# Kernel tuning notes

Measured on AMD Instinct MI355X. Metric: run time of the kernel, lower is better.

## Reference

```python
import jax, jax.numpy as jnp
import numpy as np

B, S, HID, NH = 2, 2048, 1024, 16
HD = HID // NH  # head_dim = 64


def setup_inputs() -> dict:
    key = jax.random.key(0)
    ks = jax.random.split(key, 11)
    sc = 1.0 / np.sqrt(HID)
    inp = {
        "query": jax.random.normal(ks[0], (B, S, HID), jnp.float32),
        "key_": jax.random.normal(ks[1], (B, S, HID), jnp.float32),
        "value": jax.random.normal(ks[2], (B, S, HID), jnp.float32),
        "Wq": jax.random.normal(ks[3], (HID, HID), jnp.float32) * sc,
        "bq": jnp.zeros((HID,), jnp.float32),
        "Wk": jax.random.normal(ks[4], (HID, HID), jnp.float32) * sc,
        "bk": jnp.zeros((HID,), jnp.float32),
        "Wv": jax.random.normal(ks[5], (HID, HID), jnp.float32) * sc,
        "bv": jnp.zeros((HID,), jnp.float32),
        "Wo": jax.random.normal(ks[6], (HID, HID), jnp.float32) * sc,
        "bo": jnp.zeros((HID,), jnp.float32),
    }
    return inp


def _split_heads(x):
    # [B, S, HID] -> [B, NH, S, HD]
    return x.reshape(B, S, NH, HD).transpose(0, 2, 1, 3)


def reference(query, key_, value, Wq, bq, Wk, bk, Wv, bv, Wo, bo):
    q = _split_heads(query @ Wq + bq)
    k = _split_heads(key_ @ Wk + bk)
    v = _split_heads(value @ Wv + bv)
    scale = 1.0 / jnp.sqrt(jnp.asarray(HD, q.dtype))
    # [B, NH, S, S] scores (unfused attention, as in the original module)
    scores = jnp.einsum("bhqd,bhkd->bhqk", q, k) * scale
    attn = jax.nn.softmax(scores, axis=-1)
    ctx = jnp.einsum("bhqk,bhkd->bhqd", attn, v)  # [B, NH, S, HD]
    ctx = ctx.transpose(0, 2, 1, 3).reshape(B, S, HID)
    return ctx @ Wo + bo
```

## Files before the change

kernel.cpp:

```cpp
#include <hip/hip_runtime.h>


typedef unsigned short u16;
typedef unsigned int u32;
typedef __bf16 bf16x8 __attribute__((ext_vector_type(8)));
typedef float f32x4 __attribute__((ext_vector_type(4)));
typedef u16 u16x4 __attribute__((ext_vector_type(4)));

__device__ __forceinline__ u16 f2bf(float f) {
  __bf16 h = (__bf16)f;
  return *(u16*)&h;
}

__device__ __forceinline__ void gll16(const void* g, void* l) {
  __builtin_amdgcn_global_load_lds(
      (const __attribute__((address_space(1))) u32*)g,
      (__attribute__((address_space(3))) u32*)l, 16, 0, 0);
}

__global__ __launch_bounds__(256) void prep_kernel(
    const float* __restrict__ q32, const float* __restrict__ k32,
    const float* __restrict__ v32,
    u16* __restrict__ qb, u16* __restrict__ kb, u16* __restrict__ vb,
    const float* __restrict__ W0, const float* __restrict__ W1,
    const float* __restrict__ W2, const float* __restrict__ W3,
    u16* __restrict__ T0, u16* __restrict__ T1,
    u16* __restrict__ T2, u16* __restrict__ T3) {
  int blk = blockIdx.x, tid = threadIdx.x;
  if (blk < 12288) {
    int which = blk >> 12;
    const float* in = (which == 0) ? q32 : (which == 1) ? k32 : v32;
    u16* out = (which == 0) ? qb : (which == 1) ? kb : vb;
    int i = (blk & 4095) * 256 + tid;
    float4 v = ((const float4*)in)[i];
    u16x4 o;
    o.x = f2bf(v.x); o.y = f2bf(v.y); o.z = f2bf(v.z); o.w = f2bf(v.w);
    ((u16x4*)out)[i] = o;
  } else {
    int tb = blk - 12288;
    int z = tb >> 10, rest = tb & 1023;
    const float* W = (z == 0) ? W0 : (z == 1) ? W1 : (z == 2) ? W2 : W3;
    u16* WT = (z == 0) ? T0 : (z == 1) ? T1 : (z == 2) ? T2 : T3;
    __shared__ float t[32][33];
    int bx = (rest & 31) * 32, by = (rest >> 5) * 32;
    int tx = tid & 31, ty = tid >> 5;
#pragma unroll
    for (int i = ty; i < 32; i += 8) t[i][tx] = W[(by + i) * 1024 + bx + tx];
    __syncthreads();
#pragma unroll
    for (int i = ty; i < 32; i += 8) WT[(bx + i) * 1024 + by + tx] = f2bf(t[tx][i]);
  }
}

struct GemmJob {
  const u16* A; const u16* BT; const float* bias;
  float* Cf; u16* Cb; int mode; float oscale;
};

template <int BN>
__global__ __launch_bounds__(256, 4) void gemm_sbuf(GemmJob j0, GemmJob j1, GemmJob j2) {
  constexpr int NT = BN / 32;
  constexpr int NBC = BN / 32;
  const int K = 1024, N = 1024;
  __shared__ __align__(16) u16 As[128 * 64];
  __shared__ __align__(16) u16 Bs[BN * 64];
  int blk = blockIdx.x, tid = threadIdx.x;
  int z, r0, bm, bn;
  if (BN == 128) {
    z = blk >> 8; r0 = blk & 255;
    int xcd = r0 & 7, i5 = r0 >> 3;
    bm = (xcd * 4 + (i5 & 3)) * 128;
    bn = (i5 >> 2) * 128;
  } else {
    z = 0; r0 = blk;
    int xcd = r0 & 7, i6 = r0 >> 3;
    bm = (xcd * 4 + (i6 & 3)) * 128;
    bn = (i6 >> 2) * 64;
  }
  GemmJob j = (z == 0) ? j0 : (z == 1) ? j1 : j2;
  int w = tid >> 6, lane = tid & 63, quad = lane >> 4, l16 = lane & 15;
  int wr = (w >> 1) * 64, wc = (w & 1) * (BN / 2);
  f32x4 acc[4][NT] = {};

  auto stage = [&](int kk) {
#pragma unroll
    for (int i = 0; i < 4; ++i) {
      int c = tid + i * 256;
      int r = c >> 3, jp = c & 7, jg = jp ^ (r & 7);
      gll16(&j.A[(size_t)(bm + r) * K + kk + jg * 8], &As[c * 8]);
    }
#pragma unroll
    for (int i = 0; i < NBC; ++i) {
      int c = tid + i * 256;
      int r = c >> 3, jp = c & 7, jg = jp ^ (r & 7);
      gll16(&j.BT[(size_t)(bn + r) * K + kk + jg * 8], &Bs[c * 8]);
    }
  };

  for (int it = 0; it < 16; ++it) {
    __syncthreads();
    stage(it * 64);
    __syncthreads();
#pragma unroll
    for (int ks = 0; ks < 2; ++ks) {
      bf16x8 af[4], bfr[NT];
#pragma unroll
      for (int mt = 0; mt < 4; ++mt) {
        int row = wr + mt * 16 + l16;
        af[mt] = *(const bf16x8*)&As[row * 64 + (((ks * 4 + quad) ^ (row & 7))) * 8];
      }
#pragma unroll
      for (int nt = 0; nt < NT; ++nt) {
        int row = wc + nt * 16 + l16;
        bfr[nt] = *(const bf16x8*)&Bs[row * 64 + (((ks * 4 + quad) ^ (row & 7))) * 8];
      }
#pragma unroll
      for (int mt = 0; mt < 4; ++mt)
#pragma unroll
        for (int nt = 0; nt < NT; ++nt)
          acc[mt][nt] = __builtin_amdgcn_mfma_f32_16x16x32_bf16(af[mt], bfr[nt], acc[mt][nt], 0, 0, 0);
    }
  }

#pragma unroll
  for (int mt = 0; mt < 4; ++mt)
#pragma unroll
    for (int nt = 0; nt < NT; ++nt)
#pragma unroll
      for (int r = 0; r < 4; ++r) {
        int row = bm + wr + mt * 16 + quad * 4 + r;
        int col = bn + wc + nt * 16 + l16;
        float v = (acc[mt][nt][r] + j.bias[col]) * j.oscale;
        if (j.mode == 0) {
          j.Cf[(size_t)row * N + col] = v;
        } else {
          int b = row >> 11, s = row & 2047, h = col >> 6, d = col & 63;
          u16 bv = f2bf(v);
          if (j.mode == 1)
            j.Cb[(((size_t)(b * 16 + h) * 2048 + s) << 6) + d] = bv;
          else
            j.Cb[((size_t)(b * 16 + h) * 64 + d) * 2048 + s] = bv;
        }
      }
}

__global__ __launch_bounds__(512, 4) void attn_kernel(
    const u16* __restrict__ Q,
    const u16* __restrict__ Kk,
    const u16* __restrict__ VT,
    u16* __restrict__ ctx)
{
  __shared__ __align__(16) u16 Ks[2][2][64 * 64];
  __shared__ __align__(16) u16 Vs[2][2][64 * 64];

  int blk = blockIdx.x;
  int qt = (blk >> 3) & 15;
  int bh = (blk & 7) * 4 + (blk >> 7);
  int b = bh >> 4, h = bh & 15;
  const u16* Qb = Q + ((size_t)bh * 2048 + qt * 128) * 64;
  const u16* Kb = Kk + (size_t)bh * 2048 * 64;
  const u16* Vb = VT + (size_t)bh * 64 * 2048;
  int tid = threadIdx.x, w = tid >> 6, lane = tid & 63, quad = lane >> 4, l16 = lane & 15;
  int g = tid >> 8;
  int wl = w & 3;
  int tt = tid & 255;
  int rowbase = wl * 32;

  bf16x8 qf[2][2];
#pragma unroll
  for (int f = 0; f < 2; ++f)
#pragma unroll
    for (int ks = 0; ks < 2; ++ks)
      qf[f][ks] = *(const bf16x8*)&Qb[(rowbase + f * 16 + l16) * 64 + ks * 32 + quad * 8];

  f32x4 Oacc[2][4] = {};
  float lacc0 = 0.f, lacc1 = 0.f;

  int c0 = tt, c1 = tt + 256;
  int kr0 = c0 >> 3, kj0 = (c0 & 7) ^ (kr0 & 7);
  int kr1 = c1 >> 3, kj1 = (c1 & 7) ^ (kr1 & 7);
  const u16* ksrc0 = Kb + (size_t)(g * 1024 + kr0) * 64 + kj0 * 8;
  const u16* ksrc1 = Kb + (size_t)(g * 1024 + kr1) * 64 + kj1 * 8;
  const u16* vsrc0 = Vb + (size_t)kr0 * 2048 + g * 1024 + kj0 * 8;
  const u16* vsrc1 = Vb + (size_t)kr1 * 2048 + g * 1024 + kj1 * 8;
  u16* kdst0 = &Ks[g][0][c0 * 8];
  u16* kdst1 = &Ks[g][0][c1 * 8];
  u16* vdst0 = &Vs[g][0][c0 * 8];
  u16* vdst1 = &Vs[g][0][c1 * 8];

  u32 koff[2][2][2];
  u32 voff[2][4];
#pragma unroll
  for (int c = 0; c < 2; ++c) {
#pragma unroll
    for (int nt2 = 0; nt2 < 2; ++nt2)
#pragma unroll
      for (int ks = 0; ks < 2; ++ks)
        koff[c][nt2][ks] = ((c * 2 + nt2) * 16 + l16) * 64 +
                           (((ks * 4 + quad) ^ (l16 & 7)) * 8);
#pragma unroll
    for (int dt = 0; dt < 4; ++dt)
      voff[c][dt] = (dt * 16 + l16) * 64 + ((((c * 4 + quad) ^ (l16 & 7))) * 8);
  }
  const u16* kbase = &Ks[g][0][0];
  const u16* vbase = &Vs[g][0][0];

  gll16(ksrc0, kdst0); gll16(ksrc1, kdst1);
  gll16(vsrc0, vdst0); gll16(vsrc1, vdst1);
  __syncthreads();

  for (int kv = 0; kv < 16; ++kv) {
    int cur = kv & 1;
    if (kv < 15) {
      ksrc0 += 64 * 64; ksrc1 += 64 * 64;
      vsrc0 += 64;      vsrc1 += 64;
      u32 so = (cur ^ 1) * (64 * 64);
      gll16(ksrc0, kdst0 + so); gll16(ksrc1, kdst1 + so);
      gll16(vsrc0, vdst0 + so); gll16(vsrc1, vdst1 + so);
    }
    u32 bo = cur * (64 * 64);
    const u16* kb = kbase + bo;
    const u16* vb = vbase + bo;

#pragma unroll
    for (int c = 0; c < 2; ++c) {
      f32x4 Sc[2][2] = {};
      __builtin_amdgcn_s_setprio(1);
#pragma unroll
      for (int nt2 = 0; nt2 < 2; ++nt2) {
#pragma unroll
        for (int ks = 0; ks < 2; ++ks) {
          bf16x8 kfr = *(const bf16x8*)(kb + koff[c][nt2][ks]);
          Sc[0][nt2] = __builtin_amdgcn_mfma_f32_16x16x32_bf16(kfr, qf[0][ks], Sc[0][nt2], 0, 0, 0);
          Sc[1][nt2] = __builtin_amdgcn_mfma_f32_16x16x32_bf16(kfr, qf[1][ks], Sc[1][nt2], 0, 0, 0);
        }
      }
      __builtin_amdgcn_s_setprio(0);

      bf16x8 pf[2];
#pragma unroll
      for (int f = 0; f < 2; ++f) {
        float p0 = __builtin_amdgcn_exp2f(Sc[f][0][0]);
        float p1 = __builtin_amdgcn_exp2f(Sc[f][0][1]);
        float p2 = __builtin_amdgcn_exp2f(Sc[f][0][2]);
        float p3 = __builtin_amdgcn_exp2f(Sc[f][0][3]);
        float p4 = __builtin_amdgcn_exp2f(Sc[f][1][0]);
        float p5 = __builtin_amdgcn_exp2f(Sc[f][1][1]);
        float p6 = __builtin_amdgcn_exp2f(Sc[f][1][2]);
        float p7 = __builtin_amdgcn_exp2f(Sc[f][1][3]);
        float ls = ((p0 + p1) + (p2 + p3)) + ((p4 + p5) + (p6 + p7));
        if (f == 0) lacc0 += ls; else lacc1 += ls;
        u32 u0, u1, u2, u3;
        asm("v_cvt_pk_bf16_f32 %0, %1, %2" : "=v"(u0) : "v"(p0), "v"(p1));
        asm("v_cvt_pk_bf16_f32 %0, %1, %2" : "=v"(u1) : "v"(p2), "v"(p3));
        asm("v_cvt_pk_bf16_f32 %0, %1, %2" : "=v"(u2) : "v"(p4), "v"(p5));
        asm("v_cvt_pk_bf16_f32 %0, %1, %2" : "=v"(u3) : "v"(p6), "v"(p7));
        asm("v_permlane32_swap_b32 %0, %1" : "+v"(u0), "+v"(u2));
        asm("v_permlane32_swap_b32 %0, %1" : "+v"(u1), "+v"(u3));
        asm("v_permlane16_swap_b32 %0, %1" : "+v"(u0), "+v"(u2));
        asm("v_permlane16_swap_b32 %0, %1" : "+v"(u1), "+v"(u3));
        union { u32 u[4]; bf16x8 v; } cv;
        cv.u[0] = u0; cv.u[1] = u1; cv.u[2] = u2; cv.u[3] = u3;
        pf[f] = cv.v;
      }

      __builtin_amdgcn_s_setprio(1);
#pragma unroll
      for (int dt = 0; dt < 4; ++dt) {
        bf16x8 vf = *(const bf16x8*)(vb + voff[c][dt]);
        Oacc[0][dt] = __builtin_amdgcn_mfma_f32_16x16x32_bf16(vf, pf[0], Oacc[0][dt], 0, 0, 0);
        Oacc[1][dt] = __builtin_amdgcn_mfma_f32_16x16x32_bf16(vf, pf[1], Oacc[1][dt], 0, 0, 0);
      }
      __builtin_amdgcn_s_setprio(0);
    }

    __syncthreads();
  }

  float lred[2];
#pragma unroll
  for (int f = 0; f < 2; ++f) {
    float l = (f == 0) ? lacc0 : lacc1;
    l += __shfl_xor(l, 16, 64);
    l += __shfl_xor(l, 32, 64);
    lred[f] = l;
  }

  float* ox = (float*)&Ks[0][0][0];
  float* lx = (float*)&Vs[0][0][0];
  if (g == 1) {
#pragma unroll
    for (int f = 0; f < 2; ++f) {
#pragma unroll
      for (int dt = 0; dt < 4; ++dt) {
        int jc = (dt * 4 + quad) ^ l16;
        *(f32x4*)&ox[(size_t)(rowbase + f * 16 + l16) * 64 + jc * 4] = Oacc[f][dt];
      }
      if (quad == 0) lx[rowbase + f * 16 + l16] = lred[f];
    }
  }
  __syncthreads();
  if (g == 0) {
#pragma unroll
    for (int f = 0; f < 2; ++f) {
      float lt = lred[f] + lx[rowbase + f * 16 + l16];
      float linv = 1.0f / lt;
      int s = qt * 128 + rowbase + f * 16 + l16;
#pragma unroll
      for (int dt = 0; dt < 4; ++dt) {
        int jc = (dt * 4 + quad) ^ l16;
        f32x4 o1 = *(const f32x4*)&ox[(size_t)(rowbase + f * 16 + l16) * 64 + jc * 4];
        u16x4 o;
#pragma unroll
        for (int r = 0; r < 4; ++r) o[r] = f2bf((Oacc[f][dt][r] + o1[r]) * linv);
        *(u16x4*)&ctx[(size_t)(b * 2048 + s) * 1024 + h * 64 + dt * 16 + quad * 4] = o;
      }
    }
  }
}


extern "C" void kernel_launch(void* const* d_in, const int* in_sizes, int n_in,
                              void* d_out, int out_size, void* d_ws, size_t ws_size,
                              hipStream_t stream) {
  const float* query = (const float*)d_in[0];
  const float* key_  = (const float*)d_in[1];
  const float* value = (const float*)d_in[2];
  const float* Wq = (const float*)d_in[3];
  const float* bq = (const float*)d_in[4];
  const float* Wk = (const float*)d_in[5];
  const float* bk = (const float*)d_in[6];
  const float* Wv = (const float*)d_in[7];
  const float* bv = (const float*)d_in[8];
  const float* Wo = (const float*)d_in[9];
  const float* bo = (const float*)d_in[10];
  float* out = (float*)d_out;

  char* ws = (char*)d_ws;
  const size_t MB = 1024 * 1024;
  u16* Aq  = (u16*)(ws + 0 * MB);
  u16* Ak  = (u16*)(ws + 8 * MB);
  u16* Av  = (u16*)(ws + 16 * MB);
  u16* WqT = (u16*)(ws + 24 * MB);
  u16* WkT = (u16*)(ws + 26 * MB);
  u16* WvT = (u16*)(ws + 28 * MB);
  u16* WoT = (u16*)(ws + 30 * MB);
  u16* Qp  = (u16*)(ws + 32 * MB);
  u16* Kp  = (u16*)(ws + 40 * MB);
  u16* VTp = (u16*)(ws + 48 * MB);
  u16* Ctx = (u16*)(ws + 56 * MB);

  prep_kernel<<<16384, 256, 0, stream>>>(query, key_, value, Aq, Ak, Av,
                                         Wq, Wk, Wv, Wo, WqT, WkT, WvT, WoT);

  const float sc = 0.125f * 1.44269504f;
  GemmJob jq{Aq, WqT, bq, nullptr, Qp, 1, sc};
  GemmJob jk{Ak, WkT, bk, nullptr, Kp, 1, 1.0f};
  GemmJob jv{Av, WvT, bv, nullptr, VTp, 2, 1.0f};
  gemm_sbuf<128><<<768, 256, 0, stream>>>(jq, jk, jv);

  attn_kernel<<<512, 512, 0, stream>>>(Qp, Kp, VTp, Ctx);

  GemmJob jo{Ctx, WoT, bo, out, nullptr, 0, 1.0f};
  gemm_sbuf<64><<<512, 256, 0, stream>>>(jo, jo, jo);
}
```

Baseline: 225.6 us.

## Split attention KV sequence across four wave groups with 1024-thread blocks

Doubles the attention block to 1024 threads and splits the key/value sequence into four 512-key groups instead of two, each streaming 32-key tiles with double-buffered async loads into LDS. The partial output accumulators and row sums are combined through a two-stage LDS tree reduction before normalisation and the bf16 store. This raises the number of waves in flight to hide memory and MFMA latency. It costs an extra reduction stage with more barriers, smaller tiles with more loop iterations, and register pressure under the tighter launch bounds.

```diff
diff --git a/kernel.cpp b/kernel.cpp
--- a/kernel.cpp
+++ b/kernel.cpp
@@ -144,14 +144,14 @@
       }
 }
 
-__global__ __launch_bounds__(512, 4) void attn_kernel(
+__global__ __launch_bounds__(1024, 4) void attn_kernel(
     const u16* __restrict__ Q,
     const u16* __restrict__ Kk,
     const u16* __restrict__ VT,
     u16* __restrict__ ctx)
 {
-  __shared__ __align__(16) u16 Ks[2][2][64 * 64];
-  __shared__ __align__(16) u16 Vs[2][2][64 * 64];
+  __shared__ __align__(16) u16 Ks[4][2][32 * 64];
+  __shared__ __align__(16) u16 Vs[4][2][64 * 32];
 
   int blk = blockIdx.x;
   int qt = (blk >> 3) & 15;
@@ -160,9 +160,9 @@
   const u16* Qb = Q + ((size_t)bh * 2048 + qt * 128) * 64;
   const u16* Kb = Kk + (size_t)bh * 2048 * 64;
   const u16* Vb = VT + (size_t)bh * 64 * 2048;
-  int tid = threadIdx.x, w = tid >> 6, lane = tid & 63, quad = lane >> 4, l16 = lane & 15;
+  int tid = threadIdx.x, lane = tid & 63, quad = lane >> 4, l16 = lane & 15;
   int g = tid >> 8;
-  int wl = w & 3;
+  int wl = (tid >> 6) & 3;
   int tt = tid & 255;
   int rowbase = wl * 32;
 
@@ -176,103 +176,91 @@
   f32x4 Oacc[2][4] = {};
   float lacc0 = 0.f, lacc1 = 0.f;
 
-  int c0 = tt, c1 = tt + 256;
-  int kr0 = c0 >> 3, kj0 = (c0 & 7) ^ (kr0 & 7);
-  int kr1 = c1 >> 3, kj1 = (c1 & 7) ^ (kr1 & 7);
-  const u16* ksrc0 = Kb + (size_t)(g * 1024 + kr0) * 64 + kj0 * 8;
-  const u16* ksrc1 = Kb + (size_t)(g * 1024 + kr1) * 64 + kj1 * 8;
-  const u16* vsrc0 = Vb + (size_t)kr0 * 2048 + g * 1024 + kj0 * 8;
-  const u16* vsrc1 = Vb + (size_t)kr1 * 2048 + g * 1024 + kj1 * 8;
-  u16* kdst0 = &Ks[g][0][c0 * 8];
-  u16* kdst1 = &Ks[g][0][c1 * 8];
-  u16* vdst0 = &Vs[g][0][c0 * 8];
-  u16* vdst1 = &Vs[g][0][c1 * 8];
-
-  u32 koff[2][2][2];
-  u32 voff[2][4];
-#pragma unroll
-  for (int c = 0; c < 2; ++c) {
-#pragma unroll
-    for (int nt2 = 0; nt2 < 2; ++nt2)
-#pragma unroll
-      for (int ks = 0; ks < 2; ++ks)
-        koff[c][nt2][ks] = ((c * 2 + nt2) * 16 + l16) * 64 +
-                           (((ks * 4 + quad) ^ (l16 & 7)) * 8);
-#pragma unroll
-    for (int dt = 0; dt < 4; ++dt)
-      voff[c][dt] = (dt * 16 + l16) * 64 + ((((c * 4 + quad) ^ (l16 & 7))) * 8);
-  }
+  int kr = tt >> 3, kjp = tt & 7, kjg = kjp ^ (kr & 7);
+  int vd = tt >> 2, vjp = tt & 3, vjg = vjp ^ (vd & 3);
+  const u16* ksrc = Kb + (size_t)(g * 512 + kr) * 64 + kjg * 8;
+  const u16* vsrc = Vb + (size_t)vd * 2048 + g * 512 + vjg * 8;
+  u16* kdst = &Ks[g][0][tt * 8];
+  u16* vdst = &Vs[g][0][tt * 8];
+
+  u32 koff[2][2];
+#pragma unroll
+  for (int nt2 = 0; nt2 < 2; ++nt2)
+#pragma unroll
+    for (int ks = 0; ks < 2; ++ks)
+      koff[nt2][ks] = (nt2 * 16 + l16) * 64 + (((ks * 4 + quad) ^ (l16 & 7)) * 8);
+  u32 voff[4];
+#pragma unroll
+  for (int dt = 0; dt < 4; ++dt)
+    voff[dt] = (dt * 16 + l16) * 32 + ((quad ^ (l16 & 3)) * 8);
   const u16* kbase = &Ks[g][0][0];
   const u16* vbase = &Vs[g][0][0];
 
-  gll16(ksrc0, kdst0); gll16(ksrc1, kdst1);
-  gll16(vsrc0, vdst0); gll16(vsrc1, vdst1);
+  gll16(ksrc, kdst);
+  gll16(vsrc, vdst);
   __syncthreads();
 
   for (int kv = 0; kv < 16; ++kv) {
     int cur = kv & 1;
     if (kv < 15) {
-      ksrc0 += 64 * 64; ksrc1 += 64 * 64;
-      vsrc0 += 64;      vsrc1 += 64;
-      u32 so = (cur ^ 1) * (64 * 64);
-      gll16(ksrc0, kdst0 + so); gll16(ksrc1, kdst1 + so);
-      gll16(vsrc0, vdst0 + so); gll16(vsrc1, vdst1 + so);
-    }
-    u32 bo = cur * (64 * 64);
+      ksrc += 32 * 64;
+      vsrc += 32;
+      u32 so = (cur ^ 1) * 2048;
+      gll16(ksrc, kdst + so);
+      gll16(vsrc, vdst + so);
+    }
+    u32 bo = cur * 2048;
     const u16* kb = kbase + bo;
     const u16* vb = vbase + bo;
 
-#pragma unroll
-    for (int c = 0; c < 2; ++c) {
-      f32x4 Sc[2][2] = {};
-      __builtin_amdgcn_s_setprio(1);
-#pragma unroll
-      for (int nt2 = 0; nt2 < 2; ++nt2) {
-#pragma unroll
-        for (int ks = 0; ks < 2; ++ks) {
-          bf16x8 kfr = *(const bf16x8*)(kb + koff[c][nt2][ks]);
-          Sc[0][nt2] = __builtin_amdgcn_mfma_f32_16x16x32_bf16(kfr, qf[0][ks], Sc[0][nt2], 0, 0, 0);
-          Sc[1][nt2] = __builtin_amdgcn_mfma_f32_16x16x32_bf16(kfr, qf[1][ks], Sc[1][nt2], 0, 0, 0);
-        }
-      }
-      __builtin_amdgcn_s_setprio(0);
-
-      bf16x8 pf[2];
-#pragma unroll
-      for (int f = 0; f < 2; ++f) {
-        float p0 = __builtin_amdgcn_exp2f(Sc[f][0][0]);
-        float p1 = __builtin_amdgcn_exp2f(Sc[f][0][1]);
-        float p2 = __builtin_amdgcn_exp2f(Sc[f][0][2]);
-        float p3 = __builtin_amdgcn_exp2f(Sc[f][0][3]);
-        float p4 = __builtin_amdgcn_exp2f(Sc[f][1][0]);
-        float p5 = __builtin_amdgcn_exp2f(Sc[f][1][1]);
-        float p6 = __builtin_amdgcn_exp2f(Sc[f][1][2]);
-        float p7 = __builtin_amdgcn_exp2f(Sc[f][1][3]);
-        float ls = ((p0 + p1) + (p2 + p3)) + ((p4 + p5) + (p6 + p7));
-        if (f == 0) lacc0 += ls; else lacc1 += ls;
-        u32 u0, u1, u2, u3;
-        asm("v_cvt_pk_bf16_f32 %0, %1, %2" : "=v"(u0) : "v"(p0), "v"(p1));
-        asm("v_cvt_pk_bf16_f32 %0, %1, %2" : "=v"(u1) : "v"(p2), "v"(p3));
-        asm("v_cvt_pk_bf16_f32 %0, %1, %2" : "=v"(u2) : "v"(p4), "v"(p5));
-        asm("v_cvt_pk_bf16_f32 %0, %1, %2" : "=v"(u3) : "v"(p6), "v"(p7));
-        asm("v_permlane32_swap_b32 %0, %1" : "+v"(u0), "+v"(u2));
-        asm("v_permlane32_swap_b32 %0, %1" : "+v"(u1), "+v"(u3));
-        asm("v_permlane16_swap_b32 %0, %1" : "+v"(u0), "+v"(u2));
-        asm("v_permlane16_swap_b32 %0, %1" : "+v"(u1), "+v"(u3));
-        union { u32 u[4]; bf16x8 v; } cv;
-        cv.u[0] = u0; cv.u[1] = u1; cv.u[2] = u2; cv.u[3] = u3;
-        pf[f] = cv.v;
-      }
-
-      __builtin_amdgcn_s_setprio(1);
-#pragma unroll
-      for (int dt = 0; dt < 4; ++dt) {
-        bf16x8 vf = *(const bf16x8*)(vb + voff[c][dt]);
-        Oacc[0][dt] = __builtin_amdgcn_mfma_f32_16x16x32_bf16(vf, pf[0], Oacc[0][dt], 0, 0, 0);
-        Oacc[1][dt] = __builtin_amdgcn_mfma_f32_16x16x32_bf16(vf, pf[1], Oacc[1][dt], 0, 0, 0);
-      }
-      __builtin_amdgcn_s_setprio(0);
-    }
+    f32x4 Sc[2][2] = {};
+    __builtin_amdgcn_s_setprio(1);
+#pragma unroll
+    for (int nt2 = 0; nt2 < 2; ++nt2) {
+#pragma unroll
+      for (int ks = 0; ks < 2; ++ks) {
+        bf16x8 kfr = *(const bf16x8*)(kb + koff[nt2][ks]);
+        Sc[0][nt2] = __builtin_amdgcn_mfma_f32_16x16x32_bf16(kfr, qf[0][ks], Sc[0][nt2], 0, 0, 0);
+        Sc[1][nt2] = __builtin_amdgcn_mfma_f32_16x16x32_bf16(kfr, qf[1][ks], Sc[1][nt2], 0, 0, 0);
+      }
+    }
+    __builtin_amdgcn_s_setprio(0);
+
+    bf16x8 pf[2];
+#pragma unroll
+    for (int f = 0; f < 2; ++f) {
+      float p0 = __builtin_amdgcn_exp2f(Sc[f][0][0]);
+      float p1 = __builtin_amdgcn_exp2f(Sc[f][0][1]);
+      float p2 = __builtin_amdgcn_exp2f(Sc[f][0][2]);
+      float p3 = __builtin_amdgcn_exp2f(Sc[f][0][3]);
+      float p4 = __builtin_amdgcn_exp2f(Sc[f][1][0]);
+      float p5 = __builtin_amdgcn_exp2f(Sc[f][1][1]);
+      float p6 = __builtin_amdgcn_exp2f(Sc[f][1][2]);
+      float p7 = __builtin_amdgcn_exp2f(Sc[f][1][3]);
+      float ls = ((p0 + p1) + (p2 + p3)) + ((p4 + p5) + (p6 + p7));
+      if (f == 0) lacc0 += ls; else lacc1 += ls;
+      u32 u0, u1, u2, u3;
+      asm("v_cvt_pk_bf16_f32 %0, %1, %2" : "=v"(u0) : "v"(p0), "v"(p1));
+      asm("v_cvt_pk_bf16_f32 %0, %1, %2" : "=v"(u1) : "v"(p2), "v"(p3));
+      asm("v_cvt_pk_bf16_f32 %0, %1, %2" : "=v"(u2) : "v"(p4), "v"(p5));
+      asm("v_cvt_pk_bf16_f32 %0, %1, %2" : "=v"(u3) : "v"(p6), "v"(p7));
+      asm("v_permlane32_swap_b32 %0, %1" : "+v"(u0), "+v"(u2));
+      asm("v_permlane32_swap_b32 %0, %1" : "+v"(u1), "+v"(u3));
+      asm("v_permlane16_swap_b32 %0, %1" : "+v"(u0), "+v"(u2));
+      asm("v_permlane16_swap_b32 %0, %1" : "+v"(u1), "+v"(u3));
+      union { u32 u[4]; bf16x8 v; } cv;
+      cv.u[0] = u0; cv.u[1] = u1; cv.u[2] = u2; cv.u[3] = u3;
+      pf[f] = cv.v;
+    }
+
+    __builtin_amdgcn_s_setprio(1);
+#pragma unroll
+    for (int dt = 0; dt < 4; ++dt) {
+      bf16x8 vf = *(const bf16x8*)(vb + voff[dt]);
+      Oacc[0][dt] = __builtin_amdgcn_mfma_f32_16x16x32_bf16(vf, pf[0], Oacc[0][dt], 0, 0, 0);
+      Oacc[1][dt] = __builtin_amdgcn_mfma_f32_16x16x32_bf16(vf, pf[1], Oacc[1][dt], 0, 0, 0);
+    }
+    __builtin_amdgcn_s_setprio(0);
 
     __syncthreads();
   }
@@ -286,30 +274,58 @@
     lred[f] = l;
   }
 
-  float* ox = (float*)&Ks[0][0][0];
-  float* lx = (float*)&Vs[0][0][0];
-  if (g == 1) {
-#pragma unroll
-    for (int f = 0; f < 2; ++f) {
+  float* B0 = (float*)&Ks[0][0][0];
+  float* B1 = (float*)&Vs[0][0][0];
+
+  if (g == 1 || g == 3) {
+    float* ox = (g == 1) ? B0 : B1;
+#pragma unroll
+    for (int f = 0; f < 2; ++f)
 #pragma unroll
       for (int dt = 0; dt < 4; ++dt) {
         int jc = (dt * 4 + quad) ^ l16;
         *(f32x4*)&ox[(size_t)(rowbase + f * 16 + l16) * 64 + jc * 4] = Oacc[f][dt];
       }
-      if (quad == 0) lx[rowbase + f * 16 + l16] = lred[f];
-    }
   }
   __syncthreads();
-  if (g == 0) {
-#pragma unroll
-    for (int f = 0; f < 2; ++f) {
-      float lt = lred[f] + lx[rowbase + f * 16 + l16];
-      float linv = 1.0f / lt;
-      int s = qt * 128 + rowbase + f * 16 + l16;
+  if (g == 0 || g == 2) {
+    const float* ox = (g == 0) ? B0 : B1;
+#pragma unroll
+    for (int f = 0; f < 2; ++f)
 #pragma unroll
       for (int dt = 0; dt < 4; ++dt) {
         int jc = (dt * 4 + quad) ^ l16;
         f32x4 o1 = *(const f32x4*)&ox[(size_t)(rowbase + f * 16 + l16) * 64 + jc * 4];
+        Oacc[f][dt] += o1;
+      }
+  }
+  __syncthreads();
+  if (g == 2) {
+#pragma unroll
+    for (int f = 0; f < 2; ++f)
+#pragma unroll
+      for (int dt = 0; dt < 4; ++dt) {
+        int jc = (dt * 4 + quad) ^ l16;
+        *(f32x4*)&B0[(size_t)(rowbase + f * 16 + l16) * 64 + jc * 4] = Oacc[f][dt];
+      }
+  }
+  if (g != 0 && quad == 0) {
+#pragma unroll
+    for (int f = 0; f < 2; ++f)
+      B1[(g - 1) * 128 + rowbase + f * 16 + l16] = lred[f];
+  }
+  __syncthreads();
+  if (g == 0) {
+#pragma unroll
+    for (int f = 0; f < 2; ++f) {
+      int x = rowbase + f * 16 + l16;
+      float lt = lred[f] + B1[x] + B1[128 + x] + B1[256 + x];
+      float linv = 1.0f / lt;
+      int s = qt * 128 + x;
+#pragma unroll
+      for (int dt = 0; dt < 4; ++dt) {
+        int jc = (dt * 4 + quad) ^ l16;
+        f32x4 o1 = *(const f32x4*)&B0[(size_t)x * 64 + jc * 4];
         u16x4 o;
 #pragma unroll
         for (int r = 0; r < 4; ++r) o[r] = f2bf((Oacc[f][dt][r] + o1[r]) * linv);
@@ -359,7 +375,7 @@
   GemmJob jv{Av, WvT, bv, nullptr, VTp, 2, 1.0f};
   gemm_sbuf<128><<<768, 256, 0, stream>>>(jq, jk, jv);
 
-  attn_kernel<<<512, 512, 0, stream>>>(Qp, Kp, VTp, Ctx);
+  attn_kernel<<<512, 1024, 0, stream>>>(Qp, Kp, VTp, Ctx);
 
   GemmJob jo{Ctx, WoT, bo, out, nullptr, 0, 1.0f};
   gemm_sbuf<64><<<512, 256, 0, stream>>>(jo, jo, jo);
```

New measurement: 241.4 us. 1.07x slower.
